# Optimization experiments

Hardware: AMD Instinct MI355X
Metric: run time of the kernel (lower is better)

Reference implementation:

```python
import jax, jax.numpy as jnp
import numpy as np

HEADS = 4
EPS = 1e-5

def _layernorm(x, g, b):
    mu = jnp.mean(x, axis=-1, keepdims=True)
    var = jnp.var(x, axis=-1, keepdims=True)
    return (x - mu) / jnp.sqrt(var + EPS) * g + b

def setup_inputs() -> dict:
    key = jax.random.key(0)
    ks = jax.random.split(key, 16)
    N, dim, k, G = 400000, 256, 1, 4096
    h = jax.random.normal(ks[0], (N, dim), dtype=jnp.float32)
    batch = jnp.sort(jax.random.randint(ks[1], (N,), 0, G).astype(jnp.int64))
    s = 1.0 / np.sqrt(dim)
    return {
        "h": h,
        "batch": batch,
        "num_graphs": G,
        "seed": jax.random.normal(ks[2], (k, dim), dtype=jnp.float32),
        "in_proj_w": jax.random.uniform(ks[3], (3 * dim, dim), minval=-s, maxval=s, dtype=jnp.float32),
        "in_proj_b": jnp.zeros((3 * dim,), jnp.float32),
        "out_w": jax.random.uniform(ks[4], (dim, dim), minval=-s, maxval=s, dtype=jnp.float32),
        "out_b": jnp.zeros((dim,), jnp.float32),
        "w1": jax.random.uniform(ks[5], (4 * dim, dim), minval=-s, maxval=s, dtype=jnp.float32),
        "b1": jnp.zeros((4 * dim,), jnp.float32),
        "w2": jax.random.uniform(ks[6], (dim, 4 * dim), minval=-1.0 / np.sqrt(4 * dim), maxval=1.0 / np.sqrt(4 * dim), dtype=jnp.float32),
        "b2": jnp.zeros((dim,), jnp.float32),
        "g1": jnp.ones((dim,), jnp.float32),
        "beta1": jnp.zeros((dim,), jnp.float32),
        "g2": jnp.ones((dim,), jnp.float32),
        "beta2": jnp.zeros((dim,), jnp.float32),
    }

def reference(h, batch, num_graphs, seed, in_proj_w, in_proj_b, out_w, out_b,
              w1, b1, w2, b2, g1, beta1, g2, beta2):
    N, dim = h.shape
    k = seed.shape[0]
    hd = dim // HEADS
    G = num_graphs
    # q/k/v projections (torch MHA packed in_proj: rows [0:dim]=Q, [dim:2dim]=K, [2dim:]=V)
    q = seed @ in_proj_w[:dim].T + in_proj_b[:dim]                 # [k, dim]
    kk = h @ in_proj_w[dim:2 * dim].T + in_proj_b[dim:2 * dim]     # [N, dim]
    vv = h @ in_proj_w[2 * dim:].T + in_proj_b[2 * dim:]           # [N, dim]
    qh = q.reshape(k, HEADS, hd).transpose(1, 0, 2)                # [H, k, hd]
    kh = kk.reshape(N, HEADS, hd)                                  # [N, H, hd]
    vh = vv.reshape(N, HEADS, hd)                                  # [N, H, hd]
    scale = 1.0 / np.sqrt(hd)
    scores = jnp.einsum('hkd,nhd->nhk', qh, kh) * scale            # [N, H, k]
    # segment softmax over nodes of each graph
    smax = jax.ops.segment_max(scores, batch, num_segments=G)      # [G, H, k]
    e = jnp.exp(scores - smax[batch])                              # [N, H, k]
    denom = jax.ops.segment_sum(e, batch, num_segments=G)          # [G, H, k]
    wv = jax.ops.segment_sum(e[:, :, :, None] * vh[:, :, None, :], batch, num_segments=G)  # [G, H, k, hd]
    attn = jnp.where(denom[..., None] > 0, wv / jnp.maximum(denom, 1e-9)[..., None], 0.0)
    attn = attn.transpose(0, 2, 1, 3).reshape(G, k, dim)           # [G, k, dim]
    o = attn @ out_w.T + out_b                                     # [G, k, dim]
    x = _layernorm(o + seed[None, :, :], g1, beta1)
    f = jax.nn.relu(x @ w1.T + b1) @ w2.T + b2
    x = _layernorm(x + f, g2, beta2)
    # empty graphs output zeros (matches torch loop)
    count = jax.ops.segment_sum(jnp.ones((N,), jnp.float32), batch, num_segments=G)
    return jnp.where((count > 0)[:, None, None], x, 0.0)
```

## Files before the change

kernel.cpp:

```cpp
#include <hip/hip_runtime.h>
#include <hip/hip_bf16.h>


#define DIM 256
#define CHUNK 32

typedef short bf16x8 __attribute__((ext_vector_type(8)));
typedef float f32x4  __attribute__((ext_vector_type(4)));
#define MFMA16(a, b, c) __builtin_amdgcn_mfma_f32_16x16x32_bf16(a, b, c, 0, 0, 0)

#define GLOAD_LDS16(gp, lp)                                          \
    __builtin_amdgcn_global_load_lds(                                \
        (const __attribute__((address_space(1))) void*)(gp),         \
        (__attribute__((address_space(3))) void*)(lp), 16, 0, 0)

#define OFF_C      0
#define OFF_D      1024
#define OFF_CONST  1040
#define OFF_P2B    2048
#define OFF_W1B    133120
#define OFF_W2B    264192
#define OFF_TB     395264
#define OFF_CNT    6162432
#define OFF_STARTS 6166528

__global__ __launch_bounds__(256) void prep_all_kernel(
    const float* __restrict__ seed, const float* __restrict__ ipw,
    const float* __restrict__ ipb, const float* __restrict__ out_w,
    const float* __restrict__ out_b, const float* __restrict__ w1,
    const float* __restrict__ w2, const int* __restrict__ batch,
    float* __restrict__ cvec, float* __restrict__ dconst,
    float* __restrict__ constvec, __hip_bfloat16* __restrict__ P2b,
    __hip_bfloat16* __restrict__ w1b, __hip_bfloat16* __restrict__ w2b,
    int* __restrict__ starts, int N, int G)
{
    int b = blockIdx.x, t = threadIdx.x;
    __shared__ float q_s[DIM];
    if (b < 1024) {
        int i = b >> 2, hD = b & 3;
        float a = 0.f;
        for (int j = 0; j < 64; ++j)
            a += out_w[i * DIM + hD * 64 + j]
               * ipw[(size_t)(2 * DIM + hD * 64 + j) * DIM + t];
        P2b[(size_t)i * 1024 + hD * DIM + t] = __float2bfloat16(a);
    } else if (b == 1024) {
        const float scale = 0.125f;
        float acc = ipb[t];
        for (int d = 0; d < DIM; ++d) acc += seed[d] * ipw[t * DIM + d];
        q_s[t] = acc;
        __syncthreads();
        for (int hh = 0; hh < 4; ++hh) {
            float a = 0.f;
            for (int j = 0; j < 64; ++j)
                a += q_s[hh * 64 + j] * ipw[(size_t)(DIM + hh * 64 + j) * DIM + t];
            cvec[hh * DIM + t] = a * scale;
        }
        if (t < 4) {
            float a = 0.f;
            for (int j = 0; j < 64; ++j)
                a += q_s[t * 64 + j] * ipb[DIM + t * 64 + j];
            dconst[t] = a * scale;
        }
        float cc = out_b[t];
        for (int c = 0; c < DIM; ++c)
            cc += out_w[t * DIM + c] * ipb[2 * DIM + c];
        constvec[t] = cc;
    } else if (b < 1153) {
        int base = (b - 1025) * 2048 + t;
        for (int i = 0; i < 8; ++i)
            w1b[base + i * 256] = __float2bfloat16(w1[base + i * 256]);
    } else if (b < 1281) {
        int base = (b - 1153) * 2048 + t;
        for (int i = 0; i < 8; ++i)
            w2b[base + i * 256] = __float2bfloat16(w2[base + i * 256]);
    } else {
        int n = (b - 1281) * 256 + t;
        if (n < N) {
            int bn = batch[n];
            int bp = (n == 0) ? -1 : batch[n - 1];
            for (int gg = bp + 1; gg <= bn; ++gg) starts[gg] = n;
            if (n == N - 1)
                for (int gg = bn + 1; gg <= G; ++gg) starts[gg] = N;
        }
    }
}

__global__ __launch_bounds__(256) void attn_pool_kernel(
    const float* __restrict__ hmat, const int* __restrict__ starts,
    const float* __restrict__ cvec, const float* __restrict__ dconst,
    __hip_bfloat16* __restrict__ Tb, int* __restrict__ cnt)
{
    int g = blockIdx.x;
    int tid = threadIdx.x;
    int lane = tid & 63, wave = tid >> 6;

    __shared__ float hbuf[2][CHUNK][DIM];
    __shared__ float4 esc[CHUNK];
    __shared__ float lred[4][4];

    int s = starts[g], e = starts[g + 1];
    if (tid == 0) cnt[g] = e - s;
    size_t tbase = (size_t)g * 1024;
    if (e == s) {
        __hip_bfloat16 z = __float2bfloat16(0.f);
        Tb[tbase + tid] = z; Tb[tbase + 256 + tid] = z;
        Tb[tbase + 512 + tid] = z; Tb[tbase + 768 + tid] = z;
        return;
    }

    int hh = lane & 3, seg = lane >> 2;
    const float* cb = cvec + hh * DIM + seg * 16;
    float4 cr0 = *(const float4*)(cb + 0);
    float4 cr1 = *(const float4*)(cb + 4);
    float4 cr2 = *(const float4*)(cb + 8);
    float4 cr3 = *(const float4*)(cb + 12);
    float dc_mine = dconst[hh];

    float S0 = 0.f, S1 = 0.f, S2 = 0.f, S3 = 0.f;
    float lp = 0.f;

    {
        int c0 = min(CHUNK, e - s);
#pragma unroll
        for (int i = 0; i < 8; ++i) {
            int r = wave * 8 + i;
            if (r < c0)
                GLOAD_LDS16(&hmat[(size_t)(s + r) * DIM + lane * 4],
                            &hbuf[0][r][0]);
        }
    }

    int cur = 0;
    for (int n0 = s; n0 < e; n0 += CHUNK, cur ^= 1) {
        int ccnt = min(CHUNK, e - n0);
        __syncthreads();

        int n1 = n0 + CHUNK;
        if (n1 < e) {
            int cn = min(CHUNK, e - n1);
#pragma unroll
            for (int i = 0; i < 8; ++i) {
                int r = wave * 8 + i;
                if (r < cn)
                    GLOAD_LDS16(&hmat[(size_t)(n1 + r) * DIM + lane * 4],
                                &hbuf[cur ^ 1][r][0]);
            }
        }

        for (int j = wave; j < ccnt; j += 4) {
            const float* hb = &hbuf[cur][j][seg * 16];
            float4 h0 = *(const float4*)(hb + 0);
            float4 h1 = *(const float4*)(hb + 4);
            float4 h2 = *(const float4*)(hb + 8);
            float4 h3 = *(const float4*)(hb + 12);
            float p = h0.x * cr0.x + h0.y * cr0.y + h0.z * cr0.z + h0.w * cr0.w
                    + h1.x * cr1.x + h1.y * cr1.y + h1.z * cr1.z + h1.w * cr1.w
                    + h2.x * cr2.x + h2.y * cr2.y + h2.z * cr2.z + h2.w * cr2.w
                    + h3.x * cr3.x + h3.y * cr3.y + h3.z * cr3.z + h3.w * cr3.w;
            p += __shfl_xor(p, 4);
            p += __shfl_xor(p, 8);
            p += __shfl_xor(p, 16);
            p += __shfl_xor(p, 32);
            if (lane < 4) {
                float ev = __expf(p + dc_mine);
                ((float*)&esc[j])[lane] = ev;
                lp += ev;
            }
        }
        __syncthreads();

        for (int j = 0; j < ccnt; ++j) {
            float4 e4 = esc[j];
            float hv = hbuf[cur][j][tid];
            S0 = fmaf(e4.x, hv, S0); S1 = fmaf(e4.y, hv, S1);
            S2 = fmaf(e4.z, hv, S2); S3 = fmaf(e4.w, hv, S3);
        }
    }

    __syncthreads();
    if (lane < 4) lred[wave][lane] = lp;
    __syncthreads();
    float l0 = lred[0][0] + lred[1][0] + lred[2][0] + lred[3][0];
    float l1 = lred[0][1] + lred[1][1] + lred[2][1] + lred[3][1];
    float l2 = lred[0][2] + lred[1][2] + lred[2][2] + lred[3][2];
    float l3 = lred[0][3] + lred[1][3] + lred[2][3] + lred[3][3];
    Tb[tbase + tid]       = __float2bfloat16(S0 / l0);
    Tb[tbase + 256 + tid] = __float2bfloat16(S1 / l1);
    Tb[tbase + 512 + tid] = __float2bfloat16(S2 / l2);
    Tb[tbase + 768 + tid] = __float2bfloat16(S3 / l3);
}

__global__ __launch_bounds__(256) void mlp_fused_kernel(
    const __hip_bfloat16* __restrict__ Tb, const __hip_bfloat16* __restrict__ P2b,
    const float* __restrict__ constvec, const float* __restrict__ seed,
    const float* __restrict__ g1, const float* __restrict__ be1,
    const __hip_bfloat16* __restrict__ w1b, const float* __restrict__ b1,
    const __hip_bfloat16* __restrict__ w2b, const float* __restrict__ b2,
    const float* __restrict__ g2, const float* __restrict__ be2,
    const int* __restrict__ cnt, float* __restrict__ outp)
{
    int m0 = blockIdx.x * 16;
    int tid = threadIdx.x;
    int w = tid >> 6, lane = tid & 63, quad = lane >> 4, l16 = lane & 15;

    __shared__ float x1s[16][260];
    __shared__ __hip_bfloat16 x1bs[16][264];
    __shared__ __hip_bfloat16 us[16][1032];
    __shared__ float redS[4][16], redQ[4][16];

    f32x4 acc0[4];
#pragma unroll
    for (int i = 0; i < 4; ++i) acc0[i] = (f32x4){0.f, 0.f, 0.f, 0.f};
    const __hip_bfloat16* Ap0 = Tb + (size_t)(m0 + l16) * 1024 + quad * 8;
    const __hip_bfloat16* Bp0 = P2b + (size_t)(w * 64 + l16) * 1024 + quad * 8;
    for (int k0 = 0; k0 < 1024; k0 += 32) {
        bf16x8 a = *(const bf16x8*)(Ap0 + k0);
#pragma unroll
        for (int nt = 0; nt < 4; ++nt) {
            bf16x8 b = *(const bf16x8*)(Bp0 + (size_t)nt * 16 * 1024 + k0);
            acc0[nt] = MFMA16(a, b, acc0[nt]);
        }
    }
    float v0[4][4];
    {
        float sum[4] = {0, 0, 0, 0}, sq[4] = {0, 0, 0, 0};
#pragma unroll
        for (int nt = 0; nt < 4; ++nt) {
            int col = w * 64 + nt * 16 + l16;
            float cv = constvec[col] + seed[col];
#pragma unroll
            for (int r = 0; r < 4; ++r) {
                float x = acc0[nt][r] + cv;
                v0[nt][r] = x; sum[r] += x; sq[r] += x * x;
            }
        }
#pragma unroll
        for (int r = 0; r < 4; ++r) {
            float s_ = sum[r], q_ = sq[r];
            s_ += __shfl_xor(s_, 1);  q_ += __shfl_xor(q_, 1);
            s_ += __shfl_xor(s_, 2);  q_ += __shfl_xor(q_, 2);
            s_ += __shfl_xor(s_, 4);  q_ += __shfl_xor(q_, 4);
            s_ += __shfl_xor(s_, 8);  q_ += __shfl_xor(q_, 8);
            if (l16 == 0) { redS[w][quad * 4 + r] = s_; redQ[w][quad * 4 + r] = q_; }
        }
    }
    __syncthreads();
    {
        float mu_r[4], rs_r[4];
#pragma unroll
        for (int r = 0; r < 4; ++r) {
            int row = quad * 4 + r;
            float s_ = redS[0][row] + redS[1][row] + redS[2][row] + redS[3][row];
            float q_ = redQ[0][row] + redQ[1][row] + redQ[2][row] + redQ[3][row];
            float mu = s_ * (1.f / 256);
            float var = q_ * (1.f / 256) - mu * mu;
            mu_r[r] = mu;
            rs_r[r] = rsqrtf(fmaxf(var, 0.f) + 1e-5f);
        }
#pragma unroll
        for (int nt = 0; nt < 4; ++nt) {
            int col = w * 64 + nt * 16 + l16;
            float gg = g1[col], bb = be1[col];
#pragma unroll
            for (int r = 0; r < 4; ++r) {
                int row = quad * 4 + r;
                float y = (v0[nt][r] - mu_r[r]) * rs_r[r] * gg + bb;
                x1s[row][col] = y;
                x1bs[row][col] = __float2bfloat16(y);
            }
        }
    }
    __syncthreads();

    f32x4 acc1[16];
#pragma unroll
    for (int i = 0; i < 16; ++i) acc1[i] = (f32x4){0.f, 0.f, 0.f, 0.f};
    const __hip_bfloat16* Bp1 = w1b + (size_t)(w * 256 + l16) * 256 + quad * 8;
#pragma unroll
    for (int k0 = 0; k0 < 256; k0 += 32) {
        bf16x8 a = *(const bf16x8*)&x1bs[l16][quad * 8 + k0];
#pragma unroll
        for (int nt = 0; nt < 16; ++nt) {
            bf16x8 b = *(const bf16x8*)(Bp1 + (size_t)nt * 16 * 256 + k0);
            acc1[nt] = MFMA16(a, b, acc1[nt]);
        }
    }
#pragma unroll
    for (int nt = 0; nt < 16; ++nt) {
        int col = w * 256 + nt * 16 + l16;
        float bb = b1[col];
#pragma unroll
        for (int r = 0; r < 4; ++r) {
            int row = quad * 4 + r;
            us[row][col] = __float2bfloat16(fmaxf(acc1[nt][r] + bb, 0.f));
        }
    }
    __syncthreads();

    f32x4 acc2[4];
#pragma unroll
    for (int i = 0; i < 4; ++i) acc2[i] = (f32x4){0.f, 0.f, 0.f, 0.f};
    const __hip_bfloat16* Bp2 = w2b + (size_t)(w * 64 + l16) * 1024 + quad * 8;
    for (int k0 = 0; k0 < 1024; k0 += 32) {
        bf16x8 a = *(const bf16x8*)&us[l16][quad * 8 + k0];
#pragma unroll
        for (int nt = 0; nt < 4; ++nt) {
            bf16x8 b = *(const bf16x8*)(Bp2 + (size_t)nt * 16 * 1024 + k0);
            acc2[nt] = MFMA16(a, b, acc2[nt]);
        }
    }
    float v2[4][4];
    {
        float sum[4] = {0, 0, 0, 0}, sq[4] = {0, 0, 0, 0};
#pragma unroll
        for (int nt = 0; nt < 4; ++nt) {
            int col = w * 64 + nt * 16 + l16;
            float bb = b2[col];
#pragma unroll
            for (int r = 0; r < 4; ++r) {
                int row = quad * 4 + r;
                float x = acc2[nt][r] + bb + x1s[row][col];
                v2[nt][r] = x; sum[r] += x; sq[r] += x * x;
            }
        }
#pragma unroll
        for (int r = 0; r < 4; ++r) {
            float s_ = sum[r], q_ = sq[r];
            s_ += __shfl_xor(s_, 1);  q_ += __shfl_xor(q_, 1);
            s_ += __shfl_xor(s_, 2);  q_ += __shfl_xor(q_, 2);
            s_ += __shfl_xor(s_, 4);  q_ += __shfl_xor(q_, 4);
            s_ += __shfl_xor(s_, 8);  q_ += __shfl_xor(q_, 8);
            if (l16 == 0) { redS[w][quad * 4 + r] = s_; redQ[w][quad * 4 + r] = q_; }
        }
    }
    __syncthreads();
    {
#pragma unroll
        for (int r = 0; r < 4; ++r) {
            int row = quad * 4 + r;
            float s_ = redS[0][row] + redS[1][row] + redS[2][row] + redS[3][row];
            float q_ = redQ[0][row] + redQ[1][row] + redQ[2][row] + redQ[3][row];
            float mu = s_ * (1.f / 256);
            float var = q_ * (1.f / 256) - mu * mu;
            float rs = rsqrtf(fmaxf(var, 0.f) + 1e-5f);
            int gr = m0 + row;
            float mask = (cnt[gr] > 0) ? 1.f : 0.f;
#pragma unroll
            for (int nt = 0; nt < 4; ++nt) {
                int col = w * 64 + nt * 16 + l16;
                float y = ((v2[nt][r] - mu) * rs * g2[col] + be2[col]) * mask;
                outp[(size_t)gr * 256 + col] = y;
            }
        }
    }
}

extern "C" void kernel_launch(void* const* d_in, const int* in_sizes, int n_in,
                              void* d_out, int out_size, void* d_ws, size_t ws_size,
                              hipStream_t stream) {
    const float* h     = (const float*)d_in[0];
    const int*   batch = (const int*)d_in[1];
    const float* seed  = (const float*)d_in[3];
    const float* ipw   = (const float*)d_in[4];
    const float* ipb   = (const float*)d_in[5];
    const float* out_w = (const float*)d_in[6];
    const float* out_b = (const float*)d_in[7];
    const float* w1    = (const float*)d_in[8];
    const float* b1    = (const float*)d_in[9];
    const float* w2    = (const float*)d_in[10];
    const float* b2    = (const float*)d_in[11];
    const float* g1    = (const float*)d_in[12];
    const float* be1   = (const float*)d_in[13];
    const float* g2    = (const float*)d_in[14];
    const float* be2   = (const float*)d_in[15];

    int N = in_sizes[1];
    int G = out_size / DIM;

    float* ws = (float*)d_ws;
    float* cvec     = ws + OFF_C;
    float* dconst   = ws + OFF_D;
    float* constvec = ws + OFF_CONST;
    __hip_bfloat16* P2b = (__hip_bfloat16*)(ws + OFF_P2B);
    __hip_bfloat16* w1b = (__hip_bfloat16*)(ws + OFF_W1B);
    __hip_bfloat16* w2b = (__hip_bfloat16*)(ws + OFF_W2B);
    __hip_bfloat16* Tb  = (__hip_bfloat16*)(ws + OFF_TB);
    int*   cnt      = (int*)(ws + OFF_CNT);
    int*   startsp  = (int*)(ws + OFF_STARTS);

    int sblocks = (N + 255) / 256;
    prep_all_kernel<<<1281 + sblocks, 256, 0, stream>>>(
        seed, ipw, ipb, out_w, out_b, w1, w2, batch,
        cvec, dconst, constvec, P2b, w1b, w2b, startsp, N, G);
    attn_pool_kernel<<<G, 256, 0, stream>>>(h, startsp, cvec, dconst, Tb, cnt);
    mlp_fused_kernel<<<G / 16, 256, 0, stream>>>(Tb, P2b, constvec, seed, g1, be1,
                                                 w1b, b1, w2b, b2, g2, be2, cnt,
                                                 (float*)d_out);
}
```

Measured before the change: 675.1 us.

## Accumulate weighted V per wave with shuffled exp weights, removing mid-chunk barrier

Each wave now owns the rows it scored. It broadcasts the four head exp-weights with lane shuffles and accumulates the weighted sum of h into 16 per-lane registers, instead of writing the weights to shared memory and syncing before a block-wide accumulation. Per-wave partials are reduced through shared memory once at the end. The chunk size is halved to 16 rows, which shrinks the LDS footprint and may raise occupancy. In exchange, register use rises and the global-to-LDS prefetch depth per chunk is smaller.

```diff
diff --git a/kernel.cpp b/kernel.cpp
--- a/kernel.cpp
+++ b/kernel.cpp
@@ -3,7 +3,7 @@
 
 
 #define DIM 256
-#define CHUNK 32
+#define CHUNK 16
 
 typedef short bf16x8 __attribute__((ext_vector_type(8)));
 typedef float f32x4  __attribute__((ext_vector_type(4)));
@@ -95,7 +95,6 @@
     int lane = tid & 63, wave = tid >> 6;
 
     __shared__ float hbuf[2][CHUNK][DIM];
-    __shared__ float4 esc[CHUNK];
     __shared__ float lred[4][4];
 
     int s = starts[g], e = starts[g + 1];
@@ -116,14 +115,17 @@
     float4 cr3 = *(const float4*)(cb + 12);
     float dc_mine = dconst[hh];
 
-    float S0 = 0.f, S1 = 0.f, S2 = 0.f, S3 = 0.f;
+    float S00 = 0.f, S01 = 0.f, S02 = 0.f, S03 = 0.f;
+    float S10 = 0.f, S11 = 0.f, S12 = 0.f, S13 = 0.f;
+    float S20 = 0.f, S21 = 0.f, S22 = 0.f, S23 = 0.f;
+    float S30 = 0.f, S31 = 0.f, S32 = 0.f, S33 = 0.f;
     float lp = 0.f;
 
     {
         int c0 = min(CHUNK, e - s);
 #pragma unroll
-        for (int i = 0; i < 8; ++i) {
-            int r = wave * 8 + i;
+        for (int i = 0; i < 4; ++i) {
+            int r = wave * 4 + i;
             if (r < c0)
                 GLOAD_LDS16(&hmat[(size_t)(s + r) * DIM + lane * 4],
                             &hbuf[0][r][0]);
@@ -139,8 +141,8 @@
         if (n1 < e) {
             int cn = min(CHUNK, e - n1);
 #pragma unroll
-            for (int i = 0; i < 8; ++i) {
-                int r = wave * 8 + i;
+            for (int i = 0; i < 4; ++i) {
+                int r = wave * 4 + i;
                 if (r < cn)
                     GLOAD_LDS16(&hmat[(size_t)(n1 + r) * DIM + lane * 4],
                                 &hbuf[cur ^ 1][r][0]);
@@ -148,11 +150,12 @@
         }
 
         for (int j = wave; j < ccnt; j += 4) {
-            const float* hb = &hbuf[cur][j][seg * 16];
-            float4 h0 = *(const float4*)(hb + 0);
-            float4 h1 = *(const float4*)(hb + 4);
-            float4 h2 = *(const float4*)(hb + 8);
-            float4 h3 = *(const float4*)(hb + 12);
+            const float* hb = &hbuf[cur][j][0];
+            const float* hs = hb + seg * 16;
+            float4 h0 = *(const float4*)(hs + 0);
+            float4 h1 = *(const float4*)(hs + 4);
+            float4 h2 = *(const float4*)(hs + 8);
+            float4 h3 = *(const float4*)(hs + 12);
             float p = h0.x * cr0.x + h0.y * cr0.y + h0.z * cr0.z + h0.w * cr0.w
                     + h1.x * cr1.x + h1.y * cr1.y + h1.z * cr1.z + h1.w * cr1.w
                     + h2.x * cr2.x + h2.y * cr2.y + h2.z * cr2.z + h2.w * cr2.w
@@ -161,33 +164,47 @@
             p += __shfl_xor(p, 8);
             p += __shfl_xor(p, 16);
             p += __shfl_xor(p, 32);
-            if (lane < 4) {
-                float ev = __expf(p + dc_mine);
-                ((float*)&esc[j])[lane] = ev;
-                lp += ev;
-            }
-        }
-        __syncthreads();
-
-        for (int j = 0; j < ccnt; ++j) {
-            float4 e4 = esc[j];
-            float hv = hbuf[cur][j][tid];
-            S0 = fmaf(e4.x, hv, S0); S1 = fmaf(e4.y, hv, S1);
-            S2 = fmaf(e4.z, hv, S2); S3 = fmaf(e4.w, hv, S3);
-        }
-    }
-
-    __syncthreads();
+            float ev = __expf(p + dc_mine);
+            lp += ev;
+            float e0 = __shfl(ev, 0), e1 = __shfl(ev, 1);
+            float e2 = __shfl(ev, 2), e3 = __shfl(ev, 3);
+            float v0 = hb[lane], v1 = hb[64 + lane];
+            float v2 = hb[128 + lane], v3 = hb[192 + lane];
+            S00 = fmaf(e0, v0, S00); S01 = fmaf(e0, v1, S01);
+            S02 = fmaf(e0, v2, S02); S03 = fmaf(e0, v3, S03);
+            S10 = fmaf(e1, v0, S10); S11 = fmaf(e1, v1, S11);
+            S12 = fmaf(e1, v2, S12); S13 = fmaf(e1, v3, S13);
+            S20 = fmaf(e2, v0, S20); S21 = fmaf(e2, v1, S21);
+            S22 = fmaf(e2, v2, S22); S23 = fmaf(e2, v3, S23);
+            S30 = fmaf(e3, v0, S30); S31 = fmaf(e3, v1, S31);
+            S32 = fmaf(e3, v2, S32); S33 = fmaf(e3, v3, S33);
+        }
+    }
+
+    __syncthreads();
+    float* part = &hbuf[0][0][0];
+#define PIDX(w_, h_, c_) ((((w_) * 4 + (h_)) * 4 + (c_)) * 64 + lane)
+    part[PIDX(wave, 0, 0)] = S00; part[PIDX(wave, 0, 1)] = S01;
+    part[PIDX(wave, 0, 2)] = S02; part[PIDX(wave, 0, 3)] = S03;
+    part[PIDX(wave, 1, 0)] = S10; part[PIDX(wave, 1, 1)] = S11;
+    part[PIDX(wave, 1, 2)] = S12; part[PIDX(wave, 1, 3)] = S13;
+    part[PIDX(wave, 2, 0)] = S20; part[PIDX(wave, 2, 1)] = S21;
+    part[PIDX(wave, 2, 2)] = S22; part[PIDX(wave, 2, 3)] = S23;
+    part[PIDX(wave, 3, 0)] = S30; part[PIDX(wave, 3, 1)] = S31;
+    part[PIDX(wave, 3, 2)] = S32; part[PIDX(wave, 3, 3)] = S33;
+#undef PIDX
     if (lane < 4) lred[wave][lane] = lp;
     __syncthreads();
-    float l0 = lred[0][0] + lred[1][0] + lred[2][0] + lred[3][0];
-    float l1 = lred[0][1] + lred[1][1] + lred[2][1] + lred[3][1];
-    float l2 = lred[0][2] + lred[1][2] + lred[2][2] + lred[3][2];
-    float l3 = lred[0][3] + lred[1][3] + lred[2][3] + lred[3][3];
-    Tb[tbase + tid]       = __float2bfloat16(S0 / l0);
-    Tb[tbase + 256 + tid] = __float2bfloat16(S1 / l1);
-    Tb[tbase + 512 + tid] = __float2bfloat16(S2 / l2);
-    Tb[tbase + 768 + tid] = __float2bfloat16(S3 / l3);
+
+    int cg = tid >> 6, ln = tid & 63;
+#pragma unroll
+    for (int h = 0; h < 4; ++h) {
+        int base = (h * 4 + cg) * 64 + ln;
+        float sum = part[base] + part[base + 1024]
+                  + part[base + 2048] + part[base + 3072];
+        float den = lred[0][h] + lred[1][h] + lred[2][h] + lred[3][h];
+        Tb[tbase + h * 256 + tid] = __float2bfloat16(sum / den);
+    }
 }
 
 __global__ __launch_bounds__(256) void mlp_fused_kernel(
```

Result: no change. 663.7 us (-1.7%).
